# Performance work log

Hardware: AMD Instinct MI355X
Metric: run time of the kernel (lower is better)

The kernel has to match this reference:

```python
import jax, jax.numpy as jnp
import numpy as np

N = 50000      # nodes
E = 800000     # edges
F_IN = 128     # num_features
H = 64         # hidden_dim
G = 64         # graphs in batch
EPS = 1e-5


def setup_inputs() -> dict:
    ks = jax.random.split(jax.random.key(0), 16)
    x = jax.random.normal(ks[0], (N, F_IN), dtype=jnp.float32)
    edge_index = jax.random.randint(ks[1], (2, E), 0, N, dtype=jnp.int64)
    batch = jnp.sort(jax.random.randint(ks[2], (N,), 0, G, dtype=jnp.int64))
    s = 0.05
    inp = {"x": x, "edge_index": edge_index, "batch": batch}
    # GCNConv layers: W [out,in], bias [out]; BatchNorm gamma/beta [H]
    dims = [(H, F_IN), (H, H), (H, H)]
    for i, (o, ci) in enumerate(dims):
        inp[f"W{i}"] = jax.random.normal(ks[3 + i], (o, ci), dtype=jnp.float32) * s
        inp[f"b{i}"] = jnp.zeros((o,), dtype=jnp.float32)
        inp[f"g{i}"] = jnp.ones((o,), dtype=jnp.float32)
        inp[f"be{i}"] = jnp.zeros((o,), dtype=jnp.float32)
    inp["lin1_w"] = jax.random.normal(ks[10], (H // 2, H), dtype=jnp.float32) * s
    inp["lin1_b"] = jnp.zeros((H // 2,), dtype=jnp.float32)
    inp["lin2_w"] = jax.random.normal(ks[11], (1, H // 2), dtype=jnp.float32) * s
    inp["lin2_b"] = jnp.zeros((1,), dtype=jnp.float32)
    return inp


def _gcn_conv(x, src, dst, W, b):
    # PyG GCNConv: h = x W^T; add self-loops; symmetric deg^{-1/2} norm; scatter-add; + bias
    h = x @ W.T                                   # [N, out]
    n = x.shape[0]
    deg = jax.ops.segment_sum(jnp.ones(src.shape[0], h.dtype), dst, num_segments=n) + 1.0
    dinv = jax.lax.rsqrt(deg)                     # [N]
    msg = h[src] * (dinv[src] * dinv[dst])[:, None]   # per-edge messages
    agg = jax.ops.segment_sum(msg, dst, num_segments=n)
    agg = agg + h * (dinv * dinv)[:, None]        # self-loop contribution
    return agg + b


def _bn_relu(x, g, be):
    # BatchNorm1d (training-mode batch stats, biased var) + ReLU; dropout = identity (eval)
    m = x.mean(axis=0)
    v = jnp.var(x, axis=0)
    return jax.nn.relu((x - m) * jax.lax.rsqrt(v + EPS) * g + be)


def reference(x, edge_index, batch,
              W0, b0, g0, be0, W1, b1, g1, be1, W2, b2, g2, be2,
              lin1_w, lin1_b, lin2_w, lin2_b):
    src, dst = edge_index[0], edge_index[1]
    Ws = [(W0, b0, g0, be0), (W1, b1, g1, be1), (W2, b2, g2, be2)]
    h = x
    for (W, b, g, be) in Ws:
        h = _bn_relu(_gcn_conv(h, src, dst, W, b), g, be)
    # global mean pool over graphs
    sums = jax.ops.segment_sum(h, batch, num_segments=G)          # [G, H]
    cnt = jax.ops.segment_sum(jnp.ones((h.shape[0],), h.dtype), batch, num_segments=G)
    pooled = sums / jnp.maximum(cnt, 1.0)[:, None]
    h = jax.nn.relu(pooled @ lin1_w.T + lin1_b)
    return h @ lin2_w.T + lin2_b                                   # [G, 1]
```

## Files before the change

### kernel.cpp

```cpp
#include <hip/hip_runtime.h>

#define NN 50000
#define NE 800000
#define FIN 128
#define H 64
#define NG 64
#define BN_EPS 1e-5f
#define INV_N (1.0f / 50000.0f)
#define NBKT 196

__global__ void setup_misc(const float* __restrict__ W0, const float* __restrict__ W1,
                           const float* __restrict__ W2, float* __restrict__ Wt0,
                           float* __restrict__ Wt1, float* __restrict__ Wt2,
                           float* __restrict__ sl0, float* __restrict__ sl1,
                           float* __restrict__ sl2, float* __restrict__ poolcnt,
                           int* __restrict__ bktcnt) {
    int i = blockIdx.x * 256 + threadIdx.x;
    if (i < 64 * 128) { sl0[i] = 0.f; sl1[i] = 0.f; sl2[i] = 0.f; }
    if (i < NG * H + NG) poolcnt[i] = 0.f;
    if (i < NBKT) bktcnt[i] = 0;
    if (i < FIN * 64) {
        int k = i >> 6, o = i & 63;
        Wt0[i] = W0[o * FIN + k];
    }
    if (i < H * 64) {
        int k = i >> 6, o = i & 63;
        Wt1[i] = W1[o * H + k];
        Wt2[i] = W2[o * H + k];
    }
}

__global__ void bucket_hist(const int* __restrict__ dst, int* __restrict__ bktcnt, int E) {
    __shared__ int cnt[NBKT];
    const int chunk = (E + gridDim.x - 1) / gridDim.x;
    const int e0 = blockIdx.x * chunk;
    const int e1 = min(e0 + chunk, E);
    for (int i = threadIdx.x; i < NBKT; i += 256) cnt[i] = 0;
    __syncthreads();
    for (int e = e0 + threadIdx.x; e < e1; e += 256) atomicAdd(&cnt[dst[e] >> 8], 1);
    __syncthreads();
    for (int i = threadIdx.x; i < NBKT; i += 256)
        if (cnt[i]) atomicAdd(&bktcnt[i], cnt[i]);
}

__global__ void bucket_scan(const int* __restrict__ bktcnt, int* __restrict__ bb,
                            int* __restrict__ bcur, int E) {
    __shared__ int s[256];
    int v = (threadIdx.x < NBKT) ? bktcnt[threadIdx.x] : 0;
    s[threadIdx.x] = v;
    __syncthreads();
    for (int off = 1; off < 256; off <<= 1) {
        int t = (threadIdx.x >= off) ? s[threadIdx.x - off] : 0;
        __syncthreads();
        s[threadIdx.x] += t;
        __syncthreads();
    }
    if (threadIdx.x < NBKT) {
        int base = s[threadIdx.x] - v;
        bb[threadIdx.x] = base;
        bcur[threadIdx.x] = base;
    }
    if (threadIdx.x == 0) bb[NBKT] = E;
}

__global__ void bin_edges(const int* __restrict__ src, const int* __restrict__ dst,
                          int* __restrict__ bcur, unsigned int* __restrict__ staged, int E) {
    __shared__ int cnt[NBKT];
    __shared__ int offs[NBKT];
    const int chunk = (E + gridDim.x - 1) / gridDim.x;
    const int e0 = blockIdx.x * chunk;
    const int e1 = min(e0 + chunk, E);
    for (int i = threadIdx.x; i < NBKT; i += 256) cnt[i] = 0;
    __syncthreads();
    for (int e = e0 + threadIdx.x; e < e1; e += 256) atomicAdd(&cnt[dst[e] >> 8], 1);
    __syncthreads();
    for (int i = threadIdx.x; i < NBKT; i += 256) {
        int c = cnt[i];
        offs[i] = c ? atomicAdd(&bcur[i], c) : 0;
        cnt[i] = 0;
    }
    __syncthreads();
    for (int e = e0 + threadIdx.x; e < e1; e += 256) {
        int d = dst[e];
        int bkt = d >> 8;
        int idx = atomicAdd(&cnt[bkt], 1);
        staged[offs[bkt] + idx] = (unsigned int)src[e] | ((unsigned int)(d & 255) << 16);
    }
}

__global__ void csr_build(const unsigned int* __restrict__ staged, const int* __restrict__ bb,
                          int* __restrict__ row_start, float* __restrict__ dinv,
                          int* __restrict__ csr_src, int n, int E) {
    __shared__ int cnt[256];
    __shared__ int loc[256];
    __shared__ int cur[256];
    const int b = blockIdx.x;
    cnt[threadIdx.x] = 0;
    __syncthreads();
    const int e0 = bb[b], e1 = bb[b + 1];
    for (int e = e0 + threadIdx.x; e < e1; e += 256)
        atomicAdd(&cnt[(staged[e] >> 16) & 255], 1);
    __syncthreads();
    int v = cnt[threadIdx.x];
    loc[threadIdx.x] = v;
    __syncthreads();
    for (int off = 1; off < 256; off <<= 1) {
        int t = (threadIdx.x >= off) ? loc[threadIdx.x - off] : 0;
        __syncthreads();
        loc[threadIdx.x] += t;
        __syncthreads();
    }
    const int start = e0 + loc[threadIdx.x] - v;
    const int node = b * 256 + threadIdx.x;
    if (node < n) {
        row_start[node] = start;
        dinv[node] = rsqrtf((float)v + 1.0f);
    }
    if (node == n) row_start[n] = E;
    cur[threadIdx.x] = start;
    __syncthreads();
    for (int e = e0 + threadIdx.x; e < e1; e += 256) {
        unsigned int u = staged[e];
        int j = atomicAdd(&cur[(u >> 16) & 255], 1);
        csr_src[j] = (int)(u & 0xFFFFu);
    }
}

template <int K>
__global__ __launch_bounds__(256, 4) void matmul_tile(const float* __restrict__ x,
                                                      const float* __restrict__ Wtg,
                                                      const float* __restrict__ st,
                                                      const float* __restrict__ gamma,
                                                      const float* __restrict__ beta,
                                                      float* __restrict__ out, int n) {
    __shared__ float Xs[64 * 68];
    __shared__ float Ws[64 * 64];
    const int base = blockIdx.x * 64;
    const int q = threadIdx.x >> 4;
    const int co = (threadIdx.x & 15) * 4;

    float4 a0 = make_float4(0.f, 0.f, 0.f, 0.f);
    float4 a1 = a0, a2 = a0, a3 = a0;

    for (int kc = 0; kc < K; kc += 64) {
        if (kc) __syncthreads();
        for (int i = threadIdx.x; i < 64 * 64; i += 256) Ws[i] = Wtg[kc * 64 + i];
        {
            const int kq = (threadIdx.x & 15) * 4;
            float4 sc = make_float4(1.f, 1.f, 1.f, 1.f);
            float4 sh = make_float4(0.f, 0.f, 0.f, 0.f);
            if (st) {
                int kk = kc + kq;
                float4 s = *(const float4*)&st[kk];
                float4 ss = *(const float4*)&st[64 + kk];
                float4 gm = *(const float4*)&gamma[kk];
                float4 bt = *(const float4*)&beta[kk];
                float mx = s.x * INV_N, my = s.y * INV_N, mz = s.z * INV_N, mw = s.w * INV_N;
                sc.x = gm.x * rsqrtf(ss.x * INV_N - mx * mx + BN_EPS);
                sc.y = gm.y * rsqrtf(ss.y * INV_N - my * my + BN_EPS);
                sc.z = gm.z * rsqrtf(ss.z * INV_N - mz * mz + BN_EPS);
                sc.w = gm.w * rsqrtf(ss.w * INV_N - mw * mw + BN_EPS);
                sh.x = bt.x - mx * sc.x;
                sh.y = bt.y - my * sc.y;
                sh.z = bt.z - mz * sc.z;
                sh.w = bt.w - mw * sc.w;
            }
            for (int j = 0; j < 4; ++j) {
                int r = (threadIdx.x >> 4) + j * 16;
                int row = base + r;
                float4 v = make_float4(0.f, 0.f, 0.f, 0.f);
                if (row < n) v = *(const float4*)&x[(size_t)row * K + kc + kq];
                if (st) {
                    v.x = fmaxf(v.x * sc.x + sh.x, 0.f);
                    v.y = fmaxf(v.y * sc.y + sh.y, 0.f);
                    v.z = fmaxf(v.z * sc.z + sh.z, 0.f);
                    v.w = fmaxf(v.w * sc.w + sh.w, 0.f);
                }
                *(float4*)&Xs[r * 68 + kq] = v;
            }
        }
        __syncthreads();

#pragma unroll 2
        for (int k = 0; k < 64; k += 4) {
            float4 x0 = *(const float4*)&Xs[(q + 0) * 68 + k];
            float4 x1 = *(const float4*)&Xs[(q + 16) * 68 + k];
            float4 x2 = *(const float4*)&Xs[(q + 32) * 68 + k];
            float4 x3 = *(const float4*)&Xs[(q + 48) * 68 + k];
            float4 w0 = *(const float4*)&Ws[(k + 0) * 64 + co];
            float4 w1 = *(const float4*)&Ws[(k + 1) * 64 + co];
            float4 w2 = *(const float4*)&Ws[(k + 2) * 64 + co];
            float4 w3 = *(const float4*)&Ws[(k + 3) * 64 + co];

            a0.x += x0.x * w0.x + x0.y * w1.x + x0.z * w2.x + x0.w * w3.x;
            a0.y += x0.x * w0.y + x0.y * w1.y + x0.z * w2.y + x0.w * w3.y;
            a0.z += x0.x * w0.z + x0.y * w1.z + x0.z * w2.z + x0.w * w3.z;
            a0.w += x0.x * w0.w + x0.y * w1.w + x0.z * w2.w + x0.w * w3.w;

            a1.x += x1.x * w0.x + x1.y * w1.x + x1.z * w2.x + x1.w * w3.x;
            a1.y += x1.x * w0.y + x1.y * w1.y + x1.z * w2.y + x1.w * w3.y;
            a1.z += x1.x * w0.z + x1.y * w1.z + x1.z * w2.z + x1.w * w3.z;
            a1.w += x1.x * w0.w + x1.y * w1.w + x1.z * w2.w + x1.w * w3.w;

            a2.x += x2.x * w0.x + x2.y * w1.x + x2.z * w2.x + x2.w * w3.x;
            a2.y += x2.x * w0.y + x2.y * w1.y + x2.z * w2.y + x2.w * w3.y;
            a2.z += x2.x * w0.z + x2.y * w1.z + x2.z * w2.z + x2.w * w3.z;
            a2.w += x2.x * w0.w + x2.y * w1.w + x2.z * w2.w + x2.w * w3.w;

            a3.x += x3.x * w0.x + x3.y * w1.x + x3.z * w2.x + x3.w * w3.x;
            a3.y += x3.x * w0.y + x3.y * w1.y + x3.z * w2.y + x3.w * w3.y;
            a3.z += x3.x * w0.z + x3.y * w1.z + x3.z * w2.z + x3.w * w3.z;
            a3.w += x3.x * w0.w + x3.y * w1.w + x3.z * w2.w + x3.w * w3.w;
        }
    }

    int r0 = base + q;
    if (r0 < n) *(float4*)&out[(size_t)r0 * H + co] = a0;
    if (r0 + 16 < n) *(float4*)&out[(size_t)(r0 + 16) * H + co] = a1;
    if (r0 + 32 < n) *(float4*)&out[(size_t)(r0 + 32) * H + co] = a2;
    if (r0 + 48 < n) *(float4*)&out[(size_t)(r0 + 48) * H + co] = a3;
}

__global__ void gcn_gather(const float* __restrict__ h, const int* __restrict__ row_start,
                           const int* __restrict__ csr_src, const float* __restrict__ dinv,
                           const float* __restrict__ bias, float* __restrict__ out,
                           float* __restrict__ slots, int n) {
    const int wv = threadIdx.x >> 6;
    const int c = threadIdx.x & 63;
    const int d0 = blockIdx.x * 8 + wv * 2;
    float vA = 0.f, vB = 0.f;
    if (d0 < n) {
        const int d1 = d0 + 1;
        int jA = row_start[d0];
        const int jm = row_start[d1];
        const int je = row_start[d1 + 1];
        int jB = jm;
        float diA = dinv[d0], diB = dinv[d1];
        float bA = h[(size_t)d0 * H + c] * diA * diA + bias[c];
        float bB = h[(size_t)d1 * H + c] * diB * diB + bias[c];
        float a0 = 0.f, a1 = 0.f, a2 = 0.f, a3 = 0.f;
        float b0 = 0.f, b1 = 0.f, b2 = 0.f, b3 = 0.f;
        while (jA + 4 <= jm && jB + 4 <= je) {
            int sA0 = csr_src[jA + 0], sA1 = csr_src[jA + 1];
            int sA2 = csr_src[jA + 2], sA3 = csr_src[jA + 3];
            int sB0 = csr_src[jB + 0], sB1 = csr_src[jB + 1];
            int sB2 = csr_src[jB + 2], sB3 = csr_src[jB + 3];
            float wA0 = dinv[sA0], wA1 = dinv[sA1], wA2 = dinv[sA2], wA3 = dinv[sA3];
            float wB0 = dinv[sB0], wB1 = dinv[sB1], wB2 = dinv[sB2], wB3 = dinv[sB3];
            a0 += h[(size_t)sA0 * H + c] * wA0;
            a1 += h[(size_t)sA1 * H + c] * wA1;
            a2 += h[(size_t)sA2 * H + c] * wA2;
            a3 += h[(size_t)sA3 * H + c] * wA3;
            b0 += h[(size_t)sB0 * H + c] * wB0;
            b1 += h[(size_t)sB1 * H + c] * wB1;
            b2 += h[(size_t)sB2 * H + c] * wB2;
            b3 += h[(size_t)sB3 * H + c] * wB3;
            jA += 4;
            jB += 4;
        }
        for (; jA + 4 <= jm; jA += 4) {
            int s0 = csr_src[jA + 0], s1 = csr_src[jA + 1];
            int s2 = csr_src[jA + 2], s3 = csr_src[jA + 3];
            float w0 = dinv[s0], w1 = dinv[s1], w2 = dinv[s2], w3 = dinv[s3];
            a0 += h[(size_t)s0 * H + c] * w0;
            a1 += h[(size_t)s1 * H + c] * w1;
            a2 += h[(size_t)s2 * H + c] * w2;
            a3 += h[(size_t)s3 * H + c] * w3;
        }
        for (; jA < jm; ++jA) {
            int s = csr_src[jA];
            a0 += h[(size_t)s * H + c] * dinv[s];
        }
        for (; jB + 4 <= je; jB += 4) {
            int s0 = csr_src[jB + 0], s1 = csr_src[jB + 1];
            int s2 = csr_src[jB + 2], s3 = csr_src[jB + 3];
            float w0 = dinv[s0], w1 = dinv[s1], w2 = dinv[s2], w3 = dinv[s3];
            b0 += h[(size_t)s0 * H + c] * w0;
            b1 += h[(size_t)s1 * H + c] * w1;
            b2 += h[(size_t)s2 * H + c] * w2;
            b3 += h[(size_t)s3 * H + c] * w3;
        }
        for (; jB < je; ++jB) {
            int s = csr_src[jB];
            b0 += h[(size_t)s * H + c] * dinv[s];
        }
        vA = bA + diA * ((a0 + a1) + (a2 + a3));
        vB = bB + diB * ((b0 + b1) + (b2 + b3));
        out[(size_t)d0 * H + c] = vA;
        out[(size_t)d1 * H + c] = vB;
    }
    __shared__ float ls[256], lq[256];
    ls[threadIdx.x] = vA + vB;
    lq[threadIdx.x] = vA * vA + vB * vB;
    __syncthreads();
    if (wv == 0) {
        float s = ls[c] + ls[c + 64] + ls[c + 128] + ls[c + 192];
        float q = lq[c] + lq[c + 64] + lq[c + 128] + lq[c + 192];
        float* slot = slots + (blockIdx.x & 63) * 128;
        atomicAdd(&slot[c], s);
        atomicAdd(&slot[64 + c], q);
    }
}

__global__ void reduce_slots(const float* __restrict__ slots, float* __restrict__ st) {
    int c = threadIdx.x;
    float s0 = 0.f, s1 = 0.f, s2 = 0.f, s3 = 0.f;
    for (int k = 0; k < 64; k += 4) {
        s0 += slots[(k + 0) * 128 + c];
        s1 += slots[(k + 1) * 128 + c];
        s2 += slots[(k + 2) * 128 + c];
        s3 += slots[(k + 3) * 128 + c];
    }
    st[c] = (s0 + s1) + (s2 + s3);
}

#define PROWS 16
__global__ void pool_seg(const float* __restrict__ h, const float* __restrict__ st,
                         const float* __restrict__ gamma, const float* __restrict__ beta,
                         const int* __restrict__ batch, float* __restrict__ pool,
                         float* __restrict__ cnt, int n) {
    int wave = blockIdx.x * 4 + (threadIdx.x >> 6);
    int c = threadIdx.x & 63;
    int r0 = wave * PROWS;
    if (r0 >= n) return;
    int r1 = min(r0 + PROWS, n);
    float mean = st[c] * INV_N;
    float var = st[64 + c] * INV_N - mean * mean;
    float sc = gamma[c] * rsqrtf(var + BN_EPS);
    float sh = beta[c] - mean * sc;
    int cur = batch[r0];
    float acc = 0.f;
    int nlocal = 0;
    for (int r = r0; r < r1; ++r) {
        int g = batch[r];
        if (g != cur) {
            atomicAdd(&pool[cur * H + c], acc);
            if (c == 0) atomicAdd(&cnt[cur], (float)nlocal);
            cur = g;
            acc = 0.f;
            nlocal = 0;
        }
        acc += fmaxf(h[(size_t)r * H + c] * sc + sh, 0.f);
        ++nlocal;
    }
    atomicAdd(&pool[cur * H + c], acc);
    if (c == 0) atomicAdd(&cnt[cur], (float)nlocal);
}

__global__ void final_mlp(const float* __restrict__ pool, const float* __restrict__ cnt,
                          const float* __restrict__ l1w, const float* __restrict__ l1b,
                          const float* __restrict__ l2w, const float* __restrict__ l2b,
                          float* __restrict__ out) {
    int tid = blockIdx.x * 256 + threadIdx.x;
    int g = tid >> 5;
    int j = tid & 31;
    if (g >= NG) return;
    float inv = 1.0f / fmaxf(cnt[g], 1.0f);
    float s = l1b[j];
    for (int k = 0; k < H; ++k) s += pool[g * H + k] * inv * l1w[j * H + k];
    float v = fmaxf(s, 0.0f) * l2w[j];
    for (int off = 16; off > 0; off >>= 1) v += __shfl_down(v, off, 32);
    if (j == 0) out[g] = v + l2b[0];
}

extern "C" void kernel_launch(void* const* d_in, const int* in_sizes, int n_in,
                              void* d_out, int out_size, void* d_ws, size_t ws_size,
                              hipStream_t stream) {
    const float* x = (const float*)d_in[0];
    const int* ei = (const int*)d_in[1];
    const int* batch = (const int*)d_in[2];
    const float* W[3] = {(const float*)d_in[3], (const float*)d_in[7], (const float*)d_in[11]};
    const float* b[3] = {(const float*)d_in[4], (const float*)d_in[8], (const float*)d_in[12]};
    const float* g[3] = {(const float*)d_in[5], (const float*)d_in[9], (const float*)d_in[13]};
    const float* be[3] = {(const float*)d_in[6], (const float*)d_in[10], (const float*)d_in[14]};
    const float* l1w = (const float*)d_in[15];
    const float* l1b = (const float*)d_in[16];
    const float* l2w = (const float*)d_in[17];
    const float* l2b = (const float*)d_in[18];
    float* out = (float*)d_out;

    const int* src = ei;
    const int* dst = ei + NE;

    char* wsb = (char*)d_ws;
    size_t off = 0;
    auto alloc = [&](size_t elems) {
        void* p = wsb + off;
        off += elems * 4;
        return p;
    };
    float* dinv = (float*)alloc(50048);
    float* bufA = (float*)alloc((size_t)NN * H);
    float* bufB = (float*)alloc((size_t)NN * H);
    float* slots[3] = {(float*)alloc(64 * 128), (float*)alloc(64 * 128), (float*)alloc(64 * 128)};
    float* st[3] = {(float*)alloc(128), (float*)alloc(128), (float*)alloc(128)};
    float* pool = (float*)alloc(NG * H);
    float* cnt = (float*)alloc(64);
    float* Wt[3] = {(float*)alloc(FIN * 64), (float*)alloc(H * 64), (float*)alloc(H * 64)};
    int* row_start = (int*)alloc(50112);
    int* bktcnt = (int*)alloc(256);
    int* bb = (int*)alloc(256);
    int* bcur = (int*)alloc(256);
    unsigned int* staged = (unsigned int*)alloc(NE);
    int* csr_src = (int*)alloc(NE);

    setup_misc<<<32, 256, 0, stream>>>(W[0], W[1], W[2], Wt[0], Wt[1], Wt[2], slots[0], slots[1],
                                       slots[2], pool, bktcnt);
    bucket_hist<<<256, 256, 0, stream>>>(dst, bktcnt, NE);
    bucket_scan<<<1, 256, 0, stream>>>(bktcnt, bb, bcur, NE);
    bin_edges<<<256, 256, 0, stream>>>(src, dst, bcur, staged, NE);
    csr_build<<<NBKT, 256, 0, stream>>>(staged, bb, row_start, dinv, csr_src, NN, NE);

    const int grid_mm = (NN + 63) / 64;
    const int grid_gather = (NN + 7) / 8;

    for (int L = 0; L < 3; ++L) {
        if (L == 0)
            matmul_tile<FIN><<<grid_mm, 256, 0, stream>>>(x, Wt[0], nullptr, nullptr, nullptr,
                                                          bufA, NN);
        else
            matmul_tile<H><<<grid_mm, 256, 0, stream>>>(bufB, Wt[L], st[L - 1], g[L - 1],
                                                        be[L - 1], bufA, NN);
        gcn_gather<<<grid_gather, 256, 0, stream>>>(bufA, row_start, csr_src, dinv, b[L], bufB,
                                                    slots[L], NN);
        reduce_slots<<<1, 128, 0, stream>>>(slots[L], st[L]);
    }

    const int pool_waves = (NN + PROWS - 1) / PROWS;
    pool_seg<<<(pool_waves + 3) / 4, 256, 0, stream>>>(bufB, st[2], g[2], be[2], batch, pool,
                                                       cnt, NN);
    final_mlp<<<8, 256, 0, stream>>>(pool, cnt, l1w, l1b, l2w, l2b, out);
}
```

Measured before the change: 344.7 us.

## Pre-scale by dinv in matmul, vectorize gather, fold slot reduction into consumers

The matmul epilogue now multiplies each output row by its own dinv. This lets the gather drop the per-edge dinv lookups and apply only the destination scale. The gather is rewritten so each wave handles four edges in parallel with float4 feature loads, then combines them with cross-lane shuffles. The separate reduce_slots launch is removed, and each matmul and pool block re-reduces the 64 stat slots itself, trading one launch for redundant small reads.

```diff
diff --git a/kernel.cpp b/kernel.cpp
--- a/kernel.cpp
+++ b/kernel.cpp
@@ -8,6 +8,10 @@
 #define BN_EPS 1e-5f
 #define INV_N (1.0f / 50000.0f)
 #define NBKT 196
+
+__device__ __forceinline__ void f4acc(float4& a, const float4 b) {
+    a.x += b.x; a.y += b.y; a.z += b.z; a.w += b.w;
+}
 
 __global__ void setup_misc(const float* __restrict__ W0, const float* __restrict__ W1,
                            const float* __restrict__ W2, float* __restrict__ Wt0,
@@ -129,15 +133,31 @@
 template <int K>
 __global__ __launch_bounds__(256, 4) void matmul_tile(const float* __restrict__ x,
                                                       const float* __restrict__ Wtg,
-                                                      const float* __restrict__ st,
+                                                      const float* __restrict__ slots,
                                                       const float* __restrict__ gamma,
                                                       const float* __restrict__ beta,
+                                                      const float* __restrict__ dinv,
                                                       float* __restrict__ out, int n) {
     __shared__ float Xs[64 * 68];
     __shared__ float Ws[64 * 64];
+    __shared__ __align__(16) float st_s[128];
     const int base = blockIdx.x * 64;
     const int q = threadIdx.x >> 4;
     const int co = (threadIdx.x & 15) * 4;
+
+    if (slots) {
+        if (threadIdx.x < 128) {
+            float s0 = 0.f, s1 = 0.f, s2 = 0.f, s3 = 0.f;
+            for (int k = 0; k < 64; k += 4) {
+                s0 += slots[(k + 0) * 128 + threadIdx.x];
+                s1 += slots[(k + 1) * 128 + threadIdx.x];
+                s2 += slots[(k + 2) * 128 + threadIdx.x];
+                s3 += slots[(k + 3) * 128 + threadIdx.x];
+            }
+            st_s[threadIdx.x] = (s0 + s1) + (s2 + s3);
+        }
+        __syncthreads();
+    }
 
     float4 a0 = make_float4(0.f, 0.f, 0.f, 0.f);
     float4 a1 = a0, a2 = a0, a3 = a0;
@@ -149,10 +169,10 @@
             const int kq = (threadIdx.x & 15) * 4;
             float4 sc = make_float4(1.f, 1.f, 1.f, 1.f);
             float4 sh = make_float4(0.f, 0.f, 0.f, 0.f);
-            if (st) {
+            if (slots) {
                 int kk = kc + kq;
-                float4 s = *(const float4*)&st[kk];
-                float4 ss = *(const float4*)&st[64 + kk];
+                float4 s = *(const float4*)&st_s[kk];
+                float4 ss = *(const float4*)&st_s[64 + kk];
                 float4 gm = *(const float4*)&gamma[kk];
                 float4 bt = *(const float4*)&beta[kk];
                 float mx = s.x * INV_N, my = s.y * INV_N, mz = s.z * INV_N, mw = s.w * INV_N;
@@ -170,7 +190,7 @@
                 int row = base + r;
                 float4 v = make_float4(0.f, 0.f, 0.f, 0.f);
                 if (row < n) v = *(const float4*)&x[(size_t)row * K + kc + kq];
-                if (st) {
+                if (slots) {
                     v.x = fmaxf(v.x * sc.x + sh.x, 0.f);
                     v.y = fmaxf(v.y * sc.y + sh.y, 0.f);
                     v.z = fmaxf(v.z * sc.z + sh.z, 0.f);
@@ -215,10 +235,26 @@
     }
 
     int r0 = base + q;
-    if (r0 < n) *(float4*)&out[(size_t)r0 * H + co] = a0;
-    if (r0 + 16 < n) *(float4*)&out[(size_t)(r0 + 16) * H + co] = a1;
-    if (r0 + 32 < n) *(float4*)&out[(size_t)(r0 + 32) * H + co] = a2;
-    if (r0 + 48 < n) *(float4*)&out[(size_t)(r0 + 48) * H + co] = a3;
+    if (r0 < n) {
+        float dv = dinv[r0];
+        a0.x *= dv; a0.y *= dv; a0.z *= dv; a0.w *= dv;
+        *(float4*)&out[(size_t)r0 * H + co] = a0;
+    }
+    if (r0 + 16 < n) {
+        float dv = dinv[r0 + 16];
+        a1.x *= dv; a1.y *= dv; a1.z *= dv; a1.w *= dv;
+        *(float4*)&out[(size_t)(r0 + 16) * H + co] = a1;
+    }
+    if (r0 + 32 < n) {
+        float dv = dinv[r0 + 32];
+        a2.x *= dv; a2.y *= dv; a2.z *= dv; a2.w *= dv;
+        *(float4*)&out[(size_t)(r0 + 32) * H + co] = a2;
+    }
+    if (r0 + 48 < n) {
+        float dv = dinv[r0 + 48];
+        a3.x *= dv; a3.y *= dv; a3.z *= dv; a3.w *= dv;
+        *(float4*)&out[(size_t)(r0 + 48) * H + co] = a3;
+    }
 }
 
 __global__ void gcn_gather(const float* __restrict__ h, const int* __restrict__ row_start,
@@ -226,106 +262,136 @@
                            const float* __restrict__ bias, float* __restrict__ out,
                            float* __restrict__ slots, int n) {
     const int wv = threadIdx.x >> 6;
-    const int c = threadIdx.x & 63;
+    const int lane = threadIdx.x & 63;
+    const int e = lane >> 4;
+    const int f4 = (lane & 15) * 4;
     const int d0 = blockIdx.x * 8 + wv * 2;
-    float vA = 0.f, vB = 0.f;
+    float4 scc = make_float4(0.f, 0.f, 0.f, 0.f);
+    float4 qcc = scc;
     if (d0 < n) {
         const int d1 = d0 + 1;
-        int jA = row_start[d0];
-        const int jm = row_start[d1];
-        const int je = row_start[d1 + 1];
-        int jB = jm;
-        float diA = dinv[d0], diB = dinv[d1];
-        float bA = h[(size_t)d0 * H + c] * diA * diA + bias[c];
-        float bB = h[(size_t)d1 * H + c] * diB * diB + bias[c];
-        float a0 = 0.f, a1 = 0.f, a2 = 0.f, a3 = 0.f;
-        float b0 = 0.f, b1 = 0.f, b2 = 0.f, b3 = 0.f;
-        while (jA + 4 <= jm && jB + 4 <= je) {
-            int sA0 = csr_src[jA + 0], sA1 = csr_src[jA + 1];
-            int sA2 = csr_src[jA + 2], sA3 = csr_src[jA + 3];
-            int sB0 = csr_src[jB + 0], sB1 = csr_src[jB + 1];
-            int sB2 = csr_src[jB + 2], sB3 = csr_src[jB + 3];
-            float wA0 = dinv[sA0], wA1 = dinv[sA1], wA2 = dinv[sA2], wA3 = dinv[sA3];
-            float wB0 = dinv[sB0], wB1 = dinv[sB1], wB2 = dinv[sB2], wB3 = dinv[sB3];
-            a0 += h[(size_t)sA0 * H + c] * wA0;
-            a1 += h[(size_t)sA1 * H + c] * wA1;
-            a2 += h[(size_t)sA2 * H + c] * wA2;
-            a3 += h[(size_t)sA3 * H + c] * wA3;
-            b0 += h[(size_t)sB0 * H + c] * wB0;
-            b1 += h[(size_t)sB1 * H + c] * wB1;
-            b2 += h[(size_t)sB2 * H + c] * wB2;
-            b3 += h[(size_t)sB3 * H + c] * wB3;
-            jA += 4;
-            jB += 4;
-        }
-        for (; jA + 4 <= jm; jA += 4) {
-            int s0 = csr_src[jA + 0], s1 = csr_src[jA + 1];
-            int s2 = csr_src[jA + 2], s3 = csr_src[jA + 3];
-            float w0 = dinv[s0], w1 = dinv[s1], w2 = dinv[s2], w3 = dinv[s3];
-            a0 += h[(size_t)s0 * H + c] * w0;
-            a1 += h[(size_t)s1 * H + c] * w1;
-            a2 += h[(size_t)s2 * H + c] * w2;
-            a3 += h[(size_t)s3 * H + c] * w3;
-        }
-        for (; jA < jm; ++jA) {
+        const int rA = row_start[d0];
+        const int rM = row_start[d1];
+        const int rE = row_start[d1 + 1];
+        const float dA = dinv[d0], dB = dinv[d1];
+        const float4 selfA = *(const float4*)&h[(size_t)d0 * H + f4];
+        const float4 selfB = *(const float4*)&h[(size_t)d1 * H + f4];
+        const float4 bq = *(const float4*)&bias[f4];
+        float4 a0 = make_float4(0.f, 0.f, 0.f, 0.f), a1 = a0, b0 = a0, b1 = a0;
+        int jA = rA + e;
+        int jB = rM + e;
+        while (jA + 4 < rM && jB + 4 < rE) {
+            int sA0 = csr_src[jA], sA1 = csr_src[jA + 4];
+            int sB0 = csr_src[jB], sB1 = csr_src[jB + 4];
+            f4acc(a0, *(const float4*)&h[(size_t)sA0 * H + f4]);
+            f4acc(a1, *(const float4*)&h[(size_t)sA1 * H + f4]);
+            f4acc(b0, *(const float4*)&h[(size_t)sB0 * H + f4]);
+            f4acc(b1, *(const float4*)&h[(size_t)sB1 * H + f4]);
+            jA += 8;
+            jB += 8;
+        }
+        while (jA + 4 < rM) {
+            int s0 = csr_src[jA], s1 = csr_src[jA + 4];
+            f4acc(a0, *(const float4*)&h[(size_t)s0 * H + f4]);
+            f4acc(a1, *(const float4*)&h[(size_t)s1 * H + f4]);
+            jA += 8;
+        }
+        if (jA < rM) {
             int s = csr_src[jA];
-            a0 += h[(size_t)s * H + c] * dinv[s];
-        }
-        for (; jB + 4 <= je; jB += 4) {
-            int s0 = csr_src[jB + 0], s1 = csr_src[jB + 1];
-            int s2 = csr_src[jB + 2], s3 = csr_src[jB + 3];
-            float w0 = dinv[s0], w1 = dinv[s1], w2 = dinv[s2], w3 = dinv[s3];
-            b0 += h[(size_t)s0 * H + c] * w0;
-            b1 += h[(size_t)s1 * H + c] * w1;
-            b2 += h[(size_t)s2 * H + c] * w2;
-            b3 += h[(size_t)s3 * H + c] * w3;
-        }
-        for (; jB < je; ++jB) {
+            f4acc(a0, *(const float4*)&h[(size_t)s * H + f4]);
+        }
+        while (jB + 4 < rE) {
+            int s0 = csr_src[jB], s1 = csr_src[jB + 4];
+            f4acc(b0, *(const float4*)&h[(size_t)s0 * H + f4]);
+            f4acc(b1, *(const float4*)&h[(size_t)s1 * H + f4]);
+            jB += 8;
+        }
+        if (jB < rE) {
             int s = csr_src[jB];
-            b0 += h[(size_t)s * H + c] * dinv[s];
-        }
-        vA = bA + diA * ((a0 + a1) + (a2 + a3));
-        vB = bB + diB * ((b0 + b1) + (b2 + b3));
-        out[(size_t)d0 * H + c] = vA;
-        out[(size_t)d1 * H + c] = vB;
-    }
-    __shared__ float ls[256], lq[256];
-    ls[threadIdx.x] = vA + vB;
-    lq[threadIdx.x] = vA * vA + vB * vB;
-    __syncthreads();
-    if (wv == 0) {
-        float s = ls[c] + ls[c + 64] + ls[c + 128] + ls[c + 192];
-        float q = lq[c] + lq[c + 64] + lq[c + 128] + lq[c + 192];
-        float* slot = slots + (blockIdx.x & 63) * 128;
-        atomicAdd(&slot[c], s);
-        atomicAdd(&slot[64 + c], q);
-    }
-}
-
-__global__ void reduce_slots(const float* __restrict__ slots, float* __restrict__ st) {
-    int c = threadIdx.x;
-    float s0 = 0.f, s1 = 0.f, s2 = 0.f, s3 = 0.f;
-    for (int k = 0; k < 64; k += 4) {
-        s0 += slots[(k + 0) * 128 + c];
-        s1 += slots[(k + 1) * 128 + c];
-        s2 += slots[(k + 2) * 128 + c];
-        s3 += slots[(k + 3) * 128 + c];
-    }
-    st[c] = (s0 + s1) + (s2 + s3);
+            f4acc(b0, *(const float4*)&h[(size_t)s * H + f4]);
+        }
+        f4acc(a0, a1);
+        f4acc(b0, b1);
+        a0.x += __shfl_xor(a0.x, 16); a0.x += __shfl_xor(a0.x, 32);
+        a0.y += __shfl_xor(a0.y, 16); a0.y += __shfl_xor(a0.y, 32);
+        a0.z += __shfl_xor(a0.z, 16); a0.z += __shfl_xor(a0.z, 32);
+        a0.w += __shfl_xor(a0.w, 16); a0.w += __shfl_xor(a0.w, 32);
+        b0.x += __shfl_xor(b0.x, 16); b0.x += __shfl_xor(b0.x, 32);
+        b0.y += __shfl_xor(b0.y, 16); b0.y += __shfl_xor(b0.y, 32);
+        b0.z += __shfl_xor(b0.z, 16); b0.z += __shfl_xor(b0.z, 32);
+        b0.w += __shfl_xor(b0.w, 16); b0.w += __shfl_xor(b0.w, 32);
+        float4 vA, vB;
+        vA.x = bq.x + dA * (selfA.x + a0.x);
+        vA.y = bq.y + dA * (selfA.y + a0.y);
+        vA.z = bq.z + dA * (selfA.z + a0.z);
+        vA.w = bq.w + dA * (selfA.w + a0.w);
+        vB.x = bq.x + dB * (selfB.x + b0.x);
+        vB.y = bq.y + dB * (selfB.y + b0.y);
+        vB.z = bq.z + dB * (selfB.z + b0.z);
+        vB.w = bq.w + dB * (selfB.w + b0.w);
+        if (e < 2) {
+            float4 vS;
+            vS.x = e ? vB.x : vA.x;
+            vS.y = e ? vB.y : vA.y;
+            vS.z = e ? vB.z : vA.z;
+            vS.w = e ? vB.w : vA.w;
+            *(float4*)&out[(size_t)(d0 + e) * H + f4] = vS;
+        }
+        scc.x = vA.x + vB.x; scc.y = vA.y + vB.y;
+        scc.z = vA.z + vB.z; scc.w = vA.w + vB.w;
+        qcc.x = vA.x * vA.x + vB.x * vB.x;
+        qcc.y = vA.y * vA.y + vB.y * vB.y;
+        qcc.z = vA.z * vA.z + vB.z * vB.z;
+        qcc.w = vA.w * vA.w + vB.w * vB.w;
+    }
+    __shared__ float4 reds[64], redq[64];
+    if (e == 0) {
+        reds[wv * 16 + (lane & 15)] = scc;
+        redq[wv * 16 + (lane & 15)] = qcc;
+    }
+    __syncthreads();
+    const int tid = threadIdx.x;
+    if (tid < 32) {
+        const int t = tid & 15;
+        const float4* rp = (tid < 16) ? reds : redq;
+        float4 r0 = rp[t], r1 = rp[16 + t], r2 = rp[32 + t], r3 = rp[48 + t];
+        float4 s;
+        s.x = (r0.x + r1.x) + (r2.x + r3.x);
+        s.y = (r0.y + r1.y) + (r2.y + r3.y);
+        s.z = (r0.z + r1.z) + (r2.z + r3.z);
+        s.w = (r0.w + r1.w) + (r2.w + r3.w);
+        float* slot = slots + (blockIdx.x & 63) * 128 + (tid < 16 ? 0 : 64) + t * 4;
+        atomicAdd(&slot[0], s.x);
+        atomicAdd(&slot[1], s.y);
+        atomicAdd(&slot[2], s.z);
+        atomicAdd(&slot[3], s.w);
+    }
 }
 
 #define PROWS 16
-__global__ void pool_seg(const float* __restrict__ h, const float* __restrict__ st,
+__global__ void pool_seg(const float* __restrict__ h, const float* __restrict__ slots,
                          const float* __restrict__ gamma, const float* __restrict__ beta,
                          const int* __restrict__ batch, float* __restrict__ pool,
                          float* __restrict__ cnt, int n) {
+    __shared__ __align__(16) float st_s[128];
+    if (threadIdx.x < 128) {
+        float s0 = 0.f, s1 = 0.f, s2 = 0.f, s3 = 0.f;
+        for (int k = 0; k < 64; k += 4) {
+            s0 += slots[(k + 0) * 128 + threadIdx.x];
+            s1 += slots[(k + 1) * 128 + threadIdx.x];
+            s2 += slots[(k + 2) * 128 + threadIdx.x];
+            s3 += slots[(k + 3) * 128 + threadIdx.x];
+        }
+        st_s[threadIdx.x] = (s0 + s1) + (s2 + s3);
+    }
+    __syncthreads();
     int wave = blockIdx.x * 4 + (threadIdx.x >> 6);
     int c = threadIdx.x & 63;
     int r0 = wave * PROWS;
     if (r0 >= n) return;
     int r1 = min(r0 + PROWS, n);
-    float mean = st[c] * INV_N;
-    float var = st[64 + c] * INV_N - mean * mean;
+    float mean = st_s[c] * INV_N;
+    float var = st_s[64 + c] * INV_N - mean * mean;
     float sc = gamma[c] * rsqrtf(var + BN_EPS);
     float sh = beta[c] - mean * sc;
     int cur = batch[r0];
@@ -393,7 +459,6 @@
     float* bufA = (float*)alloc((size_t)NN * H);
     float* bufB = (float*)alloc((size_t)NN * H);
     float* slots[3] = {(float*)alloc(64 * 128), (float*)alloc(64 * 128), (float*)alloc(64 * 128)};
-    float* st[3] = {(float*)alloc(128), (float*)alloc(128), (float*)alloc(128)};
     float* pool = (float*)alloc(NG * H);
     float* cnt = (float*)alloc(64);
     float* Wt[3] = {(float*)alloc(FIN * 64), (float*)alloc(H * 64), (float*)alloc(H * 64)};
@@ -417,17 +482,16 @@
     for (int L = 0; L < 3; ++L) {
         if (L == 0)
             matmul_tile<FIN><<<grid_mm, 256, 0, stream>>>(x, Wt[0], nullptr, nullptr, nullptr,
-                                                          bufA, NN);
+                                                          dinv, bufA, NN);
         else
-            matmul_tile<H><<<grid_mm, 256, 0, stream>>>(bufB, Wt[L], st[L - 1], g[L - 1],
-                                                        be[L - 1], bufA, NN);
+            matmul_tile<H><<<grid_mm, 256, 0, stream>>>(bufB, Wt[L], slots[L - 1], g[L - 1],
+                                                        be[L - 1], dinv, bufA, NN);
         gcn_gather<<<grid_gather, 256, 0, stream>>>(bufA, row_start, csr_src, dinv, b[L], bufB,
                                                     slots[L], NN);
-        reduce_slots<<<1, 128, 0, stream>>>(slots[L], st[L]);
     }
 
     const int pool_waves = (NN + PROWS - 1) / PROWS;
-    pool_seg<<<(pool_waves + 3) / 4, 256, 0, stream>>>(bufB, st[2], g[2], be[2], batch, pool,
+    pool_seg<<<(pool_waves + 3) / 4, 256, 0, stream>>>(bufB, slots[2], g[2], be[2], batch, pool,
                                                        cnt, NN);
     final_mlp<<<8, 256, 0, stream>>>(pool, cnt, l1w, l1b, l2w, l2b, out);
 }
```

After: 344.6 us. No clear change (-0.0%).
